# Performance work log

Hardware: AMD Instinct MI355X
Metric: run time of the kernel (lower is better)

Reference implementation:

```python
import jax, jax.numpy as jnp
import numpy as np

BETA = 0.25  # commitment_beta


def setup_inputs() -> dict:
    key = jax.random.key(0)
    k1, k2 = jax.random.split(key)
    x = jax.random.normal(k1, (16, 256, 32, 32), dtype=jnp.float32)
    # codebook weight: (n_embed + 1, embed_dim); last row is the padding idx (zeros)
    weight = jax.random.normal(k2, (8193, 256), dtype=jnp.float32) * 0.05
    weight = weight.at[-1].set(0.0)
    return {"x": x, "weight": weight}


def reference(x, weight):
    # Eval-mode forward of VectorQuantize2 (accept_image_fmap=True, no EMA update).
    B, C, H, W = x.shape
    xf = jnp.transpose(x, (0, 2, 3, 1)).reshape(B, H * W, C)  # b (h w) c
    emb = weight[:-1]  # [N, C], drop padding row
    # squared euclidean distance; argmin identical to torch.cdist argmin
    d2 = (
        jnp.sum(xf * xf, axis=-1, keepdims=True)
        - 2.0 * jnp.einsum("bnc,kc->bnk", xf, emb)
        + jnp.sum(emb * emb, axis=-1)
    )  # [B, HW, N]
    code = jnp.argmin(d2, axis=-1)  # [B, HW]
    x_q = emb[code]  # [B, HW, C]
    loss = BETA * jnp.mean((jax.lax.stop_gradient(x_q) - xf) ** 2) + jnp.mean(
        (x_q - jax.lax.stop_gradient(xf)) ** 2
    )
    # straight-through estimator
    xq_st = xf + jax.lax.stop_gradient(x_q - xf)
    xq_out = jnp.transpose(xq_st.reshape(B, H, W, C), (0, 3, 1, 2))  # b c h w
    code_out = code.reshape(B, H, W)
    return xq_out, loss, code_out
```

## Files before the change

### kernel.cpp

```cpp
#include <hip/hip_runtime.h>
#include <hip/hip_bf16.h>


#define N_ROWS   16384
#define KCODES   8192
#define DIM      256
#define LOSS_OFF 4194304
#define CODE_OFF 4194305
#define MARGIN_ACC 0.006f

typedef _Float16 half8  __attribute__((ext_vector_type(8)));
typedef _Float16 half4v __attribute__((ext_vector_type(4)));
typedef float    float4v __attribute__((ext_vector_type(4)));
typedef unsigned long long u64;

__device__ __forceinline__ unsigned umax32(unsigned a, unsigned b) { return a > b ? a : b; }
__device__ __forceinline__ unsigned umin32(unsigned a, unsigned b) { return a < b ? a : b; }
__device__ __forceinline__ void gll16(const _Float16* g, _Float16* l) {
  __builtin_amdgcn_global_load_lds((const __attribute__((address_space(1))) void*)g,
                                   (__attribute__((address_space(3))) void*)l, 16, 0, 0);
}


__global__ __launch_bounds__(256) void k_prep(const float* __restrict__ x, _Float16* __restrict__ xh,
                                              const float* __restrict__ wt, _Float16* __restrict__ eh,
                                              float* __restrict__ en2c,
                                              float* __restrict__ lacc, unsigned* __restrict__ cnt) {
  __shared__ __align__(16) _Float16 ls[8192];
  __shared__ float es[32];
  int t = threadIdx.x;
  if (blockIdx.x < 256) {
    if (blockIdx.x == 0 && t == 0) { *lacc = 0.f; *cnt = 0u; }
    int blk  = blockIdx.x;
    int row0 = blk * 64;
    int b    = row0 >> 10;
    int n0   = row0 & 1023;
    const float* xb = x + (size_t)b * 262144 + n0;
    _Float16 (*lsx)[72] = (_Float16(*)[72])ls;
    int c_l = t >> 2;
    int ng0 = t & 3;
    for (int cc = 0; cc < 4; ++cc) {
      if (cc) __syncthreads();
#pragma unroll
      for (int p = 0; p < 4; ++p) {
        int ng = ng0 + 4 * p;
        float4v v = *(const float4v*)&xb[(size_t)(cc * 64 + c_l) * 1024 + ng * 4];
#pragma unroll
        for (int k = 0; k < 4; ++k) lsx[ng * 4 + k][c_l] = (_Float16)v[k];
      }
      __syncthreads();
#pragma unroll
      for (int p2 = 0; p2 < 2; ++p2) {
        int unit = t + 256 * p2;
        int rl64 = unit >> 3, p7 = unit & 7;
        int r = row0 + rl64;
        int kg = p7 ^ (r & 7);
        half8 h = *(const half8*)&lsx[rl64][kg * 8];
        size_t tb = (size_t)(r >> 7) * 32768;
        *(half8*)&xh[tb + (size_t)cc * 8192 + (size_t)(r & 127) * 64 + p7 * 8] = h;
      }
    }
  } else {
    int blk  = blockIdx.x - 256;
    int lane = t & 63, wv = t >> 6;
    int k0 = blk * 32;
    const float* wb = wt + (size_t)k0 * 256;
    for (int i = 0; i < 8; ++i) {
      int lin = i * 1024 + t * 4;
      float4v v = *(const float4v*)&wb[lin];
      half4v h; float ss = 0.f;
#pragma unroll
      for (int j = 0; j < 4; ++j) { h[j] = (_Float16)v[j]; ss = fmaf(v[j], v[j], ss); }
      *(half4v*)&ls[lin] = h;
#pragma unroll
      for (int d = 32; d; d >>= 1) ss += __shfl_xor(ss, d);
      if (lane == 0) es[i * 4 + wv] = ss;
    }
    __syncthreads();
    size_t tb = (size_t)(k0 >> 7) * 32768;
    for (int i = 0; i < 4; ++i) {
      int u = i * 256 + t;
      int code_l = u >> 5;
      int cu = u & 31, chunk = cu >> 3, p = cu & 7;
      int kgl = k0 + code_l;
      int kg = p ^ (kgl & 7);
      half8 h = *(half8*)&ls[code_l * 256 + chunk * 64 + kg * 8];
      *(half8*)&eh[tb + (size_t)chunk * 8192 + (size_t)(kgl & 127) * 64 + p * 8] = h;
    }
    if (t < 32) en2c[k0 + t] = 32.0f - 0.5f * es[t];
  }
}

__global__ __launch_bounds__(256) void k_gemm(const _Float16* __restrict__ xh, const _Float16* __restrict__ eh,
                                              const float* __restrict__ en2c,
                                              u64* __restrict__ top2) {
  __shared__ __align__(16) _Float16 As[8192];
  __shared__ __align__(16) _Float16 Bs[8192];
  int t    = threadIdx.x;
  int bx   = blockIdx.x;
  int by   = blockIdx.y;
  int lane = t & 63, w = t >> 6;
  int wr = w & 1, wc = w >> 1;
  int ln15 = lane & 15, q = lane >> 4;
  int q4 = q * 4;

  const _Float16* Ag = eh + (size_t)bx * 32768;
  const _Float16* Bg = xh + (size_t)by * 32768;

  int kwave = bx * 128 + wr * 64;
  float4v cin[4];
#pragma unroll
  for (int mi = 0; mi < 4; ++mi) cin[mi] = *(const float4v*)&en2c[kwave + mi * 16 + q4];

  float4v acc[4][4];
#pragma unroll
  for (int mi = 0; mi < 4; ++mi)
#pragma unroll
    for (int ni = 0; ni < 4; ++ni) acc[mi][ni] = cin[mi];

  int so = (w * 64 + lane) * 8;
  int lo = w * 512;

  for (int ch = 0; ch < 4; ++ch) {
    if (ch) __syncthreads();
    const _Float16* ac = Ag + ch * 8192;
    const _Float16* bc = Bg + ch * 8192;
#pragma unroll
    for (int i = 0; i < 4; ++i) {
      gll16(ac + i * 2048 + so, As + i * 2048 + lo);
      gll16(bc + i * 2048 + so, Bs + i * 2048 + lo);
    }
    __syncthreads();
#pragma unroll
    for (int ks = 0; ks < 2; ++ks) {
      half8 af[4], bf[4];
#pragma unroll
      for (int mi = 0; mi < 4; ++mi) {
        int row = wr * 64 + mi * 16 + ln15;
        af[mi] = *(const half8*)&As[(row * 8 + ((ks * 4 + q) ^ (row & 7))) * 8];
      }
#pragma unroll
      for (int ni = 0; ni < 4; ++ni) {
        int row = wc * 64 + ni * 16 + ln15;
        bf[ni] = *(const half8*)&Bs[(row * 8 + ((ks * 4 + q) ^ (row & 7))) * 8];
      }
#pragma unroll
      for (int mi = 0; mi < 4; ++mi)
#pragma unroll
        for (int ni = 0; ni < 4; ++ni)
          acc[mi][ni] = __builtin_amdgcn_mfma_f32_16x16x32_f16(af[mi], bf[ni], acc[mi][ni], 0, 0, 0);
    }
  }

  __syncthreads();
  u64* ep = (u64*)(void*)As;
  int ibase = wr * 64 + q4;

#pragma unroll
  for (int ni = 0; ni < 4; ++ni) {
    unsigned hi[8], lo2[8];
#pragma unroll
    for (int j = 0; j < 8; ++j) {
      int mi = j >> 1, rb = (j & 1) * 2;
      unsigned p0 = (__float_as_uint(acc[mi][ni][rb])     & 0xFFFFFF80u) | (unsigned)(ibase + mi * 16 + rb);
      unsigned p1 = (__float_as_uint(acc[mi][ni][rb + 1]) & 0xFFFFFF80u) | (unsigned)(ibase + mi * 16 + rb + 1);
      hi[j] = umax32(p0, p1); lo2[j] = umin32(p0, p1);
    }
#pragma unroll
    for (int st = 4; st; st >>= 1)
#pragma unroll
      for (int j = 0; j < 8; ++j) if (j < st) {
        unsigned nb = umax32(hi[j], hi[j + st]);
        unsigned ns = umax32(umin32(hi[j], hi[j + st]), umax32(lo2[j], lo2[j + st]));
        hi[j] = nb; lo2[j] = ns;
      }
    unsigned b = hi[0], s = lo2[0];
#pragma unroll
    for (int d = 16; d < 64; d <<= 1) {
      unsigned ob = __shfl_xor(b, d);
      unsigned os = __shfl_xor(s, d);
      unsigned ns = umax32(umin32(b, ob), umax32(s, os));
      b = umax32(b, ob); s = ns;
    }
    if (q == 0) {
      int rl = wc * 64 + ni * 16 + ln15;
      ep[rl * 2 + wr] = ((u64)b << 32) | s;
    }
  }
  __syncthreads();
  if (t < 128) {
    u64 A = ep[t * 2 + 0], B = ep[t * 2 + 1];
    unsigned a0 = (unsigned)(A >> 32), a1 = (unsigned)A;
    unsigned b0 = (unsigned)(B >> 32), b1 = (unsigned)B;
    unsigned best = umax32(a0, b0);
    unsigned sec  = umax32(umin32(a0, b0), umax32(a1, b1));
    top2[(size_t)bx * 16384 + (size_t)by * 128 + t] = ((u64)best << 32) | sec;
  }
}

__global__ __launch_bounds__(512) void k_out(const u64* __restrict__ top2,
                                             const float* __restrict__ x, const float* __restrict__ w,
                                             float* __restrict__ out,
                                             float* __restrict__ lacc, unsigned* __restrict__ cnt) {
  __shared__ float ect[256 * 65];
  __shared__ float part[8];
  int t    = threadIdx.x;
  int lane = t & 63, wv = t >> 6;
  int blk  = blockIdx.x;
  int row0 = blk * 64;
  int b = row0 >> 10, n0 = row0 & 1023;

  for (int j = 0; j < 8; ++j) {
    int rl  = wv * 8 + j;
    int row = row0 + rl;
    u64 e = top2[(size_t)lane * 16384 + row];
    unsigned hi = (unsigned)(e >> 32), lo = (unsigned)e;
    unsigned mx = hi;
#pragma unroll
    for (int d = 1; d < 64; d <<= 1) mx = umax32(mx, __shfl_xor(mx, d));
    float fm = __uint_as_float(mx & 0xFFFFFF80u);
    float th = fm - MARGIN_ACC;
    bool c0 = __uint_as_float(hi & 0xFFFFFF80u) >= th;
    bool c1 = __uint_as_float(lo & 0xFFFFFF80u) >= th;
    u64 bal0 = __ballot(c0), bal1 = __ballot(c1);
    int kbest;
    if (__popcll(bal0) + __popcll(bal1) <= 1) {
      int l0 = __ffsll((unsigned long long)__ballot(hi == mx)) - 1;
      kbest = l0 * 128 + (int)(__shfl(hi, l0) & 127u);
    } else {
      const float* xr = x + (size_t)b * 262144 + (row & 1023);
      float4v ex;
#pragma unroll
      for (int i = 0; i < 4; ++i) ex[i] = xr[(size_t)(lane * 4 + i) * 1024];
      double bs = 1e300; int bk = 0x7fffffff;
      for (int pass = 0; pass < 2; ++pass) {
        u64 bal = pass ? bal1 : bal0;
        unsigned src = pass ? lo : hi;
        while (bal) {
          int l = __ffsll((unsigned long long)bal) - 1;
          bal &= bal - 1;
          int kc = l * 128 + (int)(__shfl(src, l) & 127u);
          float4v wv4 = *(const float4v*)&w[(size_t)kc * DIM + lane * 4];
          double s = 0.0;
#pragma unroll
          for (int i = 0; i < 4; ++i) { double ev = (double)wv4[i]; s += ev * (ev - 2.0 * (double)ex[i]); }
#pragma unroll
          for (int d = 1; d < 64; d <<= 1) s += __shfl_xor(s, d);
          if (s < bs || (s == bs && kc < bk)) { bs = s; bk = kc; }
        }
      }
      kbest = bk;
    }
    if (lane == 0) out[CODE_OFF + row] = (float)kbest;
    const float* wrow = w + (size_t)kbest * 256;
#pragma unroll
    for (int i = 0; i < 4; ++i) ect[(i * 64 + lane) * 65 + rl] = wrow[i * 64 + lane];
  }
  __syncthreads();

  float ls = 0.f;
  const size_t base = (size_t)b * 262144 + n0 + lane;
  for (int j = 0; j < 32; ++j) {
    int c = wv * 32 + j;
    float v = ect[c * 65 + lane];
    size_t a = base + (size_t)c * 1024;
    float xv = x[a];
    out[a] = v;
    float d = v - xv;
    ls = fmaf(d, d, ls);
  }
#pragma unroll
  for (int d = 32; d; d >>= 1) ls += __shfl_xor(ls, d);
  if (lane == 0) part[wv] = ls;
  __syncthreads();
  if (t == 0) {
    float s = part[0] + part[1] + part[2] + part[3] + part[4] + part[5] + part[6] + part[7];
    atomicAdd(lacc, s);
    __threadfence();
    unsigned old = atomicAdd(cnt, 1u);
    if (old == 255u) {
      __threadfence();
      out[LOSS_OFF] = 1.25f * (*(volatile float*)lacc) / 4194304.0f;
    }
  }
}

extern "C" void kernel_launch(void* const* d_in, const int* in_sizes, int n_in,
                              void* d_out, int out_size, void* d_ws, size_t ws_size,
                              hipStream_t stream) {
  const float* x = (const float*)d_in[0];
  const float* w = (const float*)d_in[1];
  float* out = (float*)d_out;
  char* ws = (char*)d_ws;
  _Float16* xh   = (_Float16*)(ws);
  _Float16* eh   = (_Float16*)(ws + 8388608);
  float*    en2c = (float*)(ws + 12582912);
  u64*      top2 = (u64*)(ws + 12615680);
  float*    lacc = (float*)(ws + 21004288);
  unsigned* cnt  = (unsigned*)(ws + 21004292);

  k_prep<<<512, 256, 0, stream>>>(x, xh, w, eh, en2c, lacc, cnt);
  k_gemm<<<dim3(64, 128), 256, 0, stream>>>(xh, eh, en2c, top2);
  k_out<<<256, 512, 0, stream>>>(top2, x, w, out, lacc, cnt);
}
```

Measured before the change: 178.1 us.

## Compute loss from GEMM distances and x-norms instead of rereading x in output

The loss is now built algebraically as sum(|x|^2) plus the per-row minimum distance term (|e|^2 - 2x·e). The x-norms are accumulated during the prep transpose, and k_out only writes the gathered codebook rows, so it no longer reads x a second time. The prep x path is also restructured to 128-row blocks with an fp32 LDS tile, and a memset replaces the in-kernel counter init. The risk is accuracy: the fast path derives the distance from an fp16 GEMM score with low bits masked off, so the loss is approximate, and it now depends on a double-precision accumulation.

```diff
diff --git a/kernel.cpp b/kernel.cpp
--- a/kernel.cpp
+++ b/kernel.cpp
@@ -24,45 +24,49 @@
 
 __global__ __launch_bounds__(256) void k_prep(const float* __restrict__ x, _Float16* __restrict__ xh,
                                               const float* __restrict__ wt, _Float16* __restrict__ eh,
-                                              float* __restrict__ en2c,
-                                              float* __restrict__ lacc, unsigned* __restrict__ cnt) {
+                                              float* __restrict__ en2c, double* __restrict__ dacc) {
+  __shared__ float lsx[128 * 65];
   __shared__ __align__(16) _Float16 ls[8192];
   __shared__ float es[32];
   int t = threadIdx.x;
-  if (blockIdx.x < 256) {
-    if (blockIdx.x == 0 && t == 0) { *lacc = 0.f; *cnt = 0u; }
+  int lane = t & 63, wv = t >> 6;
+  if (blockIdx.x < 128) {
     int blk  = blockIdx.x;
-    int row0 = blk * 64;
+    int row0 = blk * 128;
     int b    = row0 >> 10;
     int n0   = row0 & 1023;
     const float* xb = x + (size_t)b * 262144 + n0;
-    _Float16 (*lsx)[72] = (_Float16(*)[72])ls;
-    int c_l = t >> 2;
-    int ng0 = t & 3;
+    int n_l = t & 127, cg = t >> 7;
+    float sxx = 0.f;
     for (int cc = 0; cc < 4; ++cc) {
       if (cc) __syncthreads();
-#pragma unroll
-      for (int p = 0; p < 4; ++p) {
-        int ng = ng0 + 4 * p;
-        float4v v = *(const float4v*)&xb[(size_t)(cc * 64 + c_l) * 1024 + ng * 4];
-#pragma unroll
-        for (int k = 0; k < 4; ++k) lsx[ng * 4 + k][c_l] = (_Float16)v[k];
+      for (int j = 0; j < 32; ++j) {
+        int c = cc * 64 + cg * 32 + j;
+        float v = xb[(size_t)c * 1024 + n_l];
+        sxx = fmaf(v, v, sxx);
+        lsx[n_l * 65 + (c & 63)] = v;
       }
       __syncthreads();
 #pragma unroll
-      for (int p2 = 0; p2 < 2; ++p2) {
-        int unit = t + 256 * p2;
-        int rl64 = unit >> 3, p7 = unit & 7;
-        int r = row0 + rl64;
-        int kg = p7 ^ (r & 7);
-        half8 h = *(const half8*)&lsx[rl64][kg * 8];
-        size_t tb = (size_t)(r >> 7) * 32768;
-        *(half8*)&xh[tb + (size_t)cc * 8192 + (size_t)(r & 127) * 64 + p7 * 8] = h;
-      }
-    }
+      for (int i = 0; i < 4; ++i) {
+        int unit = i * 256 + t;
+        int rl = unit >> 3, p = unit & 7;
+        const float* src = &lsx[rl * 65 + p * 8];
+        half8 h;
+#pragma unroll
+        for (int k2 = 0; k2 < 8; ++k2) h[k2] = (_Float16)src[k2];
+        int p7 = p ^ (rl & 7);
+        *(half8*)&xh[(size_t)blk * 32768 + (size_t)cc * 8192 + (size_t)rl * 64 + p7 * 8] = h;
+      }
+    }
+#pragma unroll
+    for (int d = 32; d; d >>= 1) sxx += __shfl_xor(sxx, d);
+    __syncthreads();
+    if (lane == 0) lsx[wv] = sxx;
+    __syncthreads();
+    if (t == 0) atomicAdd(&dacc[0], (double)(lsx[0] + lsx[1] + lsx[2] + lsx[3]));
   } else {
-    int blk  = blockIdx.x - 256;
-    int lane = t & 63, wv = t >> 6;
+    int blk  = blockIdx.x - 128;
     int k0 = blk * 32;
     const float* wb = wt + (size_t)k0 * 256;
     for (int i = 0; i < 8; ++i) {
@@ -201,15 +205,16 @@
 __global__ __launch_bounds__(512) void k_out(const u64* __restrict__ top2,
                                              const float* __restrict__ x, const float* __restrict__ w,
                                              float* __restrict__ out,
-                                             float* __restrict__ lacc, unsigned* __restrict__ cnt) {
+                                             double* __restrict__ dacc, unsigned* __restrict__ cnt) {
   __shared__ float ect[256 * 65];
-  __shared__ float part[8];
+  __shared__ double dpart[8];
   int t    = threadIdx.x;
   int lane = t & 63, wv = t >> 6;
   int blk  = blockIdx.x;
   int row0 = blk * 64;
   int b = row0 >> 10, n0 = row0 & 1023;
 
+  double dsum = 0.0;
   for (int j = 0; j < 8; ++j) {
     int rl  = wv * 8 + j;
     int row = row0 + rl;
@@ -224,9 +229,11 @@
     bool c1 = __uint_as_float(lo & 0xFFFFFF80u) >= th;
     u64 bal0 = __ballot(c0), bal1 = __ballot(c1);
     int kbest;
+    double d2c;
     if (__popcll(bal0) + __popcll(bal1) <= 1) {
       int l0 = __ffsll((unsigned long long)__ballot(hi == mx)) - 1;
       kbest = l0 * 128 + (int)(__shfl(hi, l0) & 127u);
+      d2c = 64.0 - 2.0 * (double)fm;
     } else {
       const float* xr = x + (size_t)b * 262144 + (row & 1023);
       float4v ex;
@@ -250,37 +257,32 @@
         }
       }
       kbest = bk;
-    }
-    if (lane == 0) out[CODE_OFF + row] = (float)kbest;
+      d2c = bs;
+    }
+    if (lane == 0) { out[CODE_OFF + row] = (float)kbest; dsum += d2c; }
     const float* wrow = w + (size_t)kbest * 256;
 #pragma unroll
     for (int i = 0; i < 4; ++i) ect[(i * 64 + lane) * 65 + rl] = wrow[i * 64 + lane];
   }
   __syncthreads();
 
-  float ls = 0.f;
   const size_t base = (size_t)b * 262144 + n0 + lane;
   for (int j = 0; j < 32; ++j) {
     int c = wv * 32 + j;
-    float v = ect[c * 65 + lane];
-    size_t a = base + (size_t)c * 1024;
-    float xv = x[a];
-    out[a] = v;
-    float d = v - xv;
-    ls = fmaf(d, d, ls);
-  }
-#pragma unroll
-  for (int d = 32; d; d >>= 1) ls += __shfl_xor(ls, d);
-  if (lane == 0) part[wv] = ls;
+    out[base + (size_t)c * 1024] = ect[c * 65 + lane];
+  }
+  if (lane == 0) dpart[wv] = dsum;
   __syncthreads();
   if (t == 0) {
-    float s = part[0] + part[1] + part[2] + part[3] + part[4] + part[5] + part[6] + part[7];
-    atomicAdd(lacc, s);
+    double s = dpart[0] + dpart[1] + dpart[2] + dpart[3] + dpart[4] + dpart[5] + dpart[6] + dpart[7];
+    atomicAdd(&dacc[1], s);
     __threadfence();
     unsigned old = atomicAdd(cnt, 1u);
     if (old == 255u) {
       __threadfence();
-      out[LOSS_OFF] = 1.25f * (*(volatile float*)lacc) / 4194304.0f;
+      double sxx = *(volatile double*)&dacc[0];
+      double sd2 = *(volatile double*)&dacc[1];
+      out[LOSS_OFF] = (float)(1.25 * (sxx + sd2) / 4194304.0);
     }
   }
 }
@@ -296,10 +298,11 @@
   _Float16* eh   = (_Float16*)(ws + 8388608);
   float*    en2c = (float*)(ws + 12582912);
   u64*      top2 = (u64*)(ws + 12615680);
-  float*    lacc = (float*)(ws + 21004288);
-  unsigned* cnt  = (unsigned*)(ws + 21004292);
-
-  k_prep<<<512, 256, 0, stream>>>(x, xh, w, eh, en2c, lacc, cnt);
+  double*   dacc = (double*)(ws + 21004288);
+  unsigned* cnt  = (unsigned*)(ws + 21004304);
+
+  hipMemsetAsync(dacc, 0, 24, stream);
+  k_prep<<<384, 256, 0, stream>>>(x, xh, w, eh, en2c, dacc);
   k_gemm<<<dim3(64, 128), 256, 0, stream>>>(xh, eh, en2c, top2);
-  k_out<<<256, 512, 0, stream>>>(top2, x, w, out, lacc, cnt);
-}
+  k_out<<<256, 512, 0, stream>>>(top2, x, w, out, dacc, cnt);
+}
```

After: 180.0 us. Within noise of the previous version (+1.0%).
